# Performance work log

Hardware: AMD Instinct MI355X
Metric: run time of the kernel (lower is better)

## Reference

```python
import jax, jax.numpy as jnp
import numpy as np

B, ENC, DEC, H, W = 8, 64, 128, 128, 128
NEG = -1e30  # masked-softmax fill


def _neighbors(x):
    """x: [B,H,W,C] -> [B,H,W,9,C] 3x3 neighborhood gather (zeros at borders)."""
    b, h, w, c = x.shape
    p = jnp.pad(x, ((0, 0), (1, 1), (1, 1), (0, 0)))
    return jnp.stack([p[:, r:r + h, c_:c_ + w, :] for r in range(3) for c_ in range(3)], axis=3)


def _neighbor_mask(h, w):
    """[H,W,9] bool: which of the 9 neighbors are in-bounds per pixel."""
    m = jnp.pad(jnp.ones((h, w), dtype=bool), ((1, 1), (1, 1)))
    return jnp.stack([m[r:r + h, c_:c_ + w] for r in range(3) for c_ in range(3)], axis=2)


def setup_inputs() -> dict:
    key = jax.random.key(0)
    ks = jax.random.split(key, 12)
    s = 0.05
    return {
        "encoder_features": jax.random.normal(ks[0], (B, ENC, H, W), jnp.float32),
        "decoder_features": jax.random.normal(ks[1], (B, DEC, H, W), jnp.float32),
        "W_enc": jax.random.normal(ks[2], (ENC, ENC), jnp.float32) * s,
        "b_enc": jax.random.normal(ks[3], (ENC,), jnp.float32) * s,
        "W_dec": jax.random.normal(ks[4], (DEC, ENC), jnp.float32) * s,
        "b_dec": jax.random.normal(ks[5], (ENC,), jnp.float32) * s,
        "W_agg": jax.random.normal(ks[6], (ENC, 1), jnp.float32) * s,
        "b_agg": jax.random.normal(ks[7], (1,), jnp.float32) * s,
        "W_attn": jax.random.normal(ks[8], (2 * ENC, ENC), jnp.float32) * s,
        "b_attn": jax.random.normal(ks[9], (ENC,), jnp.float32) * s,
        "conv_w": jax.random.normal(ks[10], (3, 3, DEC, ENC), jnp.float32) * s,  # HWIO
        "conv_b": jax.random.normal(ks[11], (ENC,), jnp.float32) * s,
    }


def reference(encoder_features, decoder_features, W_enc, b_enc, W_dec, b_dec,
              W_agg, b_agg, W_attn, b_attn, conv_w, conv_b):
    # NCHW -> NHWC (format_linear)
    enc = jnp.transpose(encoder_features, (0, 2, 3, 1))  # [B,H,W,ENC]
    dec = jnp.transpose(decoder_features, (0, 2, 3, 1))  # [B,H,W,DEC]

    q = dec @ W_dec + b_dec  # [B,H,W,ENC]
    k = enc @ W_enc + b_enc  # [B,H,W,ENC]
    vals = jax.lax.conv_general_dilated(
        dec, conv_w, window_strides=(1, 1), padding='SAME',
        dimension_numbers=('NHWC', 'HWIO', 'NHWC')) + conv_b  # [B,H,W,ENC]

    kn = _neighbors(k)    # [B,H,W,9,ENC]
    en = _neighbors(enc)  # [B,H,W,9,ENC]
    mask = _neighbor_mask(q.shape[1], q.shape[2])  # [H,W,9]

    # per-neighbor additive score: agg_encoder(tanh(query + key)) -> scalar
    scores = jnp.squeeze(jnp.tanh(q[:, :, :, None, :] + kn) @ W_agg, -1) + b_agg  # [B,H,W,9]
    scores = jnp.where(mask, scores, NEG)
    attn_w = jax.nn.softmax(scores, axis=-1)  # softmax over valid neighbors only
    attn_vec = jnp.einsum('bhwn,bhwnc->bhwc', attn_w, en)  # weighted sum of raw encoder feats

    cat = jnp.concatenate([vals, attn_vec], axis=-1)  # [B,H,W,2*ENC]
    out = cat @ W_attn + b_attn
    out = jnp.where(out >= 0, out, 0.2 * out)  # LeakyReLU(0.2)
    return jnp.transpose(out, (0, 3, 1, 2))  # back to NCHW
```

## Files before the change

### kernel.cpp

```cpp
#include <hip/hip_runtime.h>

#define BB 8
#define ENC_C 64
#define DEC_C 128
#define HH 128
#define WW 128

typedef unsigned short ushort_t;
typedef __attribute__((ext_vector_type(8))) short short8;
typedef __attribute__((ext_vector_type(4))) float f32x4;

static __device__ __forceinline__ ushort_t f2bf(float x) {
  unsigned int u = __builtin_bit_cast(unsigned int, x);
  u += 0x7fff + ((u >> 16) & 1);
  return (ushort_t)(u >> 16);
}
static __device__ __forceinline__ float bf2f(ushort_t v) {
  unsigned int u = ((unsigned int)v) << 16;
  return __builtin_bit_cast(float, u);
}

__global__ __launch_bounds__(64) void pack_w_kernel(
    const float* __restrict__ conv_w, const float* __restrict__ W_attn,
    const float* __restrict__ W_dec, const float* __restrict__ W_enc,
    ushort_t* __restrict__ packedC, ushort_t* __restrict__ packedA,
    ushort_t* __restrict__ packedQ, ushort_t* __restrict__ packedK)
{
  const int blk = blockIdx.x;
  const int l = threadIdx.x;
  const float* W;
  ushort_t* dst;
  int bb;
  if (blk < 144) {
    const int kstep = blk >> 2, nf = blk & 3;
    const int tap = kstep >> 2, dstep = kstep & 3;
    const int n = nf * 16 + (l & 15);
    const int dbase = dstep * 32 + (l >> 4) * 8;
    ushort_t v[8];
    #pragma unroll
    for (int j = 0; j < 8; ++j)
      v[j] = f2bf(conv_w[(tap * DEC_C + dbase + j) * 64 + n]);
    ushort_t* d = packedC + ((long)blk * 64 + l) * 8;
    #pragma unroll
    for (int j = 0; j < 8; ++j) d[j] = v[j];
    return;
  } else if (blk < 160) {
    W = W_attn; dst = packedA; bb = blk - 144;
  } else if (blk < 176) {
    W = W_dec;  dst = packedQ; bb = blk - 160;
  } else {
    W = W_enc;  dst = packedK; bb = blk - 176;
  }
  const int ks = bb >> 2, nf = bb & 3;
  const int n = nf * 16 + (l & 15);
  const int kbase = ks * 32 + (l >> 4) * 8;
  ushort_t v[8];
  #pragma unroll
  for (int j = 0; j < 8; ++j)
    v[j] = f2bf(W[(kbase + j) * 64 + n]);
  ushort_t* d = dst + ((long)bb * 64 + l) * 8;
  #pragma unroll
  for (int j = 0; j < 8; ++j) d[j] = v[j];
}

__global__ __launch_bounds__(256) void prep_kernel(
    const float* __restrict__ enc, const float* __restrict__ dec,
    const ushort_t* __restrict__ packedQ, const ushort_t* __restrict__ packedK,
    const float* __restrict__ b_enc, const float* __restrict__ b_dec,
    ushort_t* __restrict__ q_nhwc, ushort_t* __restrict__ k_nhwc,
    ushort_t* __restrict__ enc_t, ushort_t* __restrict__ dec_t)
{
  __shared__ float smem[WW * 68];
  const int bh = blockIdx.x;
  const int b = bh >> 7, h = bh & 127;
  const int tid = threadIdx.x;
  const int l = tid & 63;
  const int wv = tid >> 6;
  const int pix0 = wv * 32;
  const int col = l & 15, kg = l >> 4;

  #pragma unroll
  for (int i = 0; i < 32; ++i) {
    int idx = tid + i * 256;
    int cc = idx >> 7, wl = idx & 127;
    smem[wl * 68 + cc] = enc[((b * ENC_C + cc) * HH + h) * WW + wl];
  }
  __syncthreads();

  #pragma unroll
  for (int i = 0; i < 32; ++i) {
    int idx = tid + i * 256;
    int wl = idx >> 6, cc = idx & 63;
    enc_t[((long)bh * WW + wl) * 64 + cc] = f2bf(smem[wl * 68 + cc]);
  }

  f32x4 acck[2][4];
  #pragma unroll
  for (int mf = 0; mf < 2; ++mf)
    #pragma unroll
    for (int nf = 0; nf < 4; ++nf)
      acck[mf][nf] = (f32x4){0.f, 0.f, 0.f, 0.f};

  #pragma unroll
  for (int ks = 0; ks < 2; ++ks) {
    short8 afr[2];
    #pragma unroll
    for (int mf = 0; mf < 2; ++mf) {
      const int pix = pix0 + mf * 16 + col;
      const float4* p = (const float4*)&smem[pix * 68 + ks * 32 + kg * 8];
      float4 x0 = p[0], x1 = p[1];
      short8 v;
      v[0] = (short)f2bf(x0.x); v[1] = (short)f2bf(x0.y);
      v[2] = (short)f2bf(x0.z); v[3] = (short)f2bf(x0.w);
      v[4] = (short)f2bf(x1.x); v[5] = (short)f2bf(x1.y);
      v[6] = (short)f2bf(x1.z); v[7] = (short)f2bf(x1.w);
      afr[mf] = v;
    }
    #pragma unroll
    for (int nf = 0; nf < 4; ++nf) {
      const short8 bfr =
          *(const short8*)(packedK + ((long)(ks * 4 + nf) * 64 + l) * 8);
      acck[0][nf] = __builtin_amdgcn_mfma_f32_16x16x32_bf16(
          afr[0], bfr, acck[0][nf], 0, 0, 0);
      acck[1][nf] = __builtin_amdgcn_mfma_f32_16x16x32_bf16(
          afr[1], bfr, acck[1][nf], 0, 0, 0);
    }
  }
  #pragma unroll
  for (int mf = 0; mf < 2; ++mf)
    #pragma unroll
    for (int nf = 0; nf < 4; ++nf)
      #pragma unroll
      for (int r = 0; r < 4; ++r) {
        const int pix = pix0 + mf * 16 + kg * 4 + r;
        const int c = nf * 16 + col;
        k_nhwc[((long)bh * WW + pix) * 64 + c] = f2bf(acck[mf][nf][r] + b_enc[c]);
      }
  __syncthreads();

  f32x4 accq[2][4];
  #pragma unroll
  for (int mf = 0; mf < 2; ++mf)
    #pragma unroll
    for (int nf = 0; nf < 4; ++nf)
      accq[mf][nf] = (f32x4){0.f, 0.f, 0.f, 0.f};

  #pragma unroll
  for (int hf = 0; hf < 2; ++hf) {
    #pragma unroll
    for (int i = 0; i < 32; ++i) {
      int idx = tid + i * 256;
      int cc = idx >> 7, wl = idx & 127;
      smem[wl * 68 + cc] = dec[((b * DEC_C + hf * 64 + cc) * HH + h) * WW + wl];
    }
    __syncthreads();

    #pragma unroll
    for (int i = 0; i < 32; ++i) {
      int idx = tid + i * 256;
      int wl = idx >> 6, cc = idx & 63;
      dec_t[((long)bh * WW + wl) * DEC_C + hf * 64 + cc] =
          f2bf(smem[wl * 68 + cc]);
    }

    #pragma unroll
    for (int ks2 = 0; ks2 < 2; ++ks2) {
      const int ks = hf * 2 + ks2;
      short8 afr[2];
      #pragma unroll
      for (int mf = 0; mf < 2; ++mf) {
        const int pix = pix0 + mf * 16 + col;
        const float4* p = (const float4*)&smem[pix * 68 + ks2 * 32 + kg * 8];
        float4 x0 = p[0], x1 = p[1];
        short8 v;
        v[0] = (short)f2bf(x0.x); v[1] = (short)f2bf(x0.y);
        v[2] = (short)f2bf(x0.z); v[3] = (short)f2bf(x0.w);
        v[4] = (short)f2bf(x1.x); v[5] = (short)f2bf(x1.y);
        v[6] = (short)f2bf(x1.z); v[7] = (short)f2bf(x1.w);
        afr[mf] = v;
      }
      #pragma unroll
      for (int nf = 0; nf < 4; ++nf) {
        const short8 bfr =
            *(const short8*)(packedQ + ((long)(ks * 4 + nf) * 64 + l) * 8);
        accq[0][nf] = __builtin_amdgcn_mfma_f32_16x16x32_bf16(
            afr[0], bfr, accq[0][nf], 0, 0, 0);
        accq[1][nf] = __builtin_amdgcn_mfma_f32_16x16x32_bf16(
            afr[1], bfr, accq[1][nf], 0, 0, 0);
      }
    }
    __syncthreads();
  }

  #pragma unroll
  for (int mf = 0; mf < 2; ++mf)
    #pragma unroll
    for (int nf = 0; nf < 4; ++nf)
      #pragma unroll
      for (int r = 0; r < 4; ++r) {
        const int pix = pix0 + mf * 16 + kg * 4 + r;
        const int c = nf * 16 + col;
        q_nhwc[((long)bh * WW + pix) * 64 + c] = f2bf(accq[mf][nf][r] + b_dec[c]);
      }
}

__global__ __launch_bounds__(256) void attn_kernel(
    const ushort_t* __restrict__ q_nhwc, const ushort_t* __restrict__ k_nhwc,
    const ushort_t* __restrict__ enc_t, const float* __restrict__ W_agg,
    const float* __restrict__ b_agg, ushort_t* __restrict__ att)
{
  const int nwg = gridDim.x;
  const int cpx = nwg >> 3;
  const int bid = blockIdx.x;
  const int swz = (bid & 7) * cpx + (bid >> 3);
  const int t = swz * 256 + threadIdx.x;
  const int pix = t >> 2;
  const int cb = (t & 3) * 16;
  const int h = (pix >> 7) & 127;
  const int w = pix & 127;

  int off[9]; bool valid[9];
  #pragma unroll
  for (int n = 0; n < 9; ++n) {
    const int dh = n / 3 - 1, dw = n % 3 - 1;
    const int nh = h + dh, nw = w + dw;
    valid[n] = (nh >= 0 && nh < HH && nw >= 0 && nw < WW);
    const int nhc = min(max(nh, 0), HH - 1);
    const int nwc = min(max(nw, 0), WW - 1);
    off[n] = (pix & ~16383) + nhc * WW + nwc;
  }

  const short8* qp = (const short8*)(q_nhwc + ((long)pix << 6) + cb);
  const short8 qa = qp[0], qb = qp[1];

  float wa[16];
  {
    float4 w0 = *(const float4*)(W_agg + cb);
    float4 w1 = *(const float4*)(W_agg + cb + 4);
    float4 w2 = *(const float4*)(W_agg + cb + 8);
    float4 w3 = *(const float4*)(W_agg + cb + 12);
    wa[0]=w0.x; wa[1]=w0.y; wa[2]=w0.z; wa[3]=w0.w;
    wa[4]=w1.x; wa[5]=w1.y; wa[6]=w1.z; wa[7]=w1.w;
    wa[8]=w2.x; wa[9]=w2.y; wa[10]=w2.z; wa[11]=w2.w;
    wa[12]=w3.x; wa[13]=w3.y; wa[14]=w3.z; wa[15]=w3.w;
  }

  float s[9];
  #pragma unroll
  for (int n = 0; n < 9; ++n) {
    const short8* kp = (const short8*)(k_nhwc + ((long)off[n] << 6) + cb);
    const short8 ka = kp[0], kb = kp[1];
    float sc = 0.f;
    #pragma unroll
    for (int e = 0; e < 8; ++e) {
      float x = bf2f((ushort_t)qa[e]) + bf2f((ushort_t)ka[e]);
      x = fminf(fmaxf(x, -15.f), 15.f);
      float z = __builtin_amdgcn_exp2f(x * 2.88539008f);
      float tt = __builtin_fmaf(-2.f, __builtin_amdgcn_rcpf(z + 1.f), 1.f);
      sc = __builtin_fmaf(tt, wa[e], sc);
    }
    #pragma unroll
    for (int e = 0; e < 8; ++e) {
      float x = bf2f((ushort_t)qb[e]) + bf2f((ushort_t)kb[e]);
      x = fminf(fmaxf(x, -15.f), 15.f);
      float z = __builtin_amdgcn_exp2f(x * 2.88539008f);
      float tt = __builtin_fmaf(-2.f, __builtin_amdgcn_rcpf(z + 1.f), 1.f);
      sc = __builtin_fmaf(tt, wa[8 + e], sc);
    }
    s[n] = sc;
  }

  #pragma unroll
  for (int n = 0; n < 9; ++n) {
    s[n] += __shfl_xor(s[n], 1);
    s[n] += __shfl_xor(s[n], 2);
  }

  const float bagg = b_agg[0];
  float m = -1e30f;
  #pragma unroll
  for (int n = 0; n < 9; ++n) {
    s[n] = valid[n] ? (s[n] + bagg) : -1e30f;
    m = fmaxf(m, s[n]);
  }
  float attw[9]; float denom = 0.f;
  #pragma unroll
  for (int n = 0; n < 9; ++n) {
    attw[n] = __builtin_amdgcn_exp2f((s[n] - m) * 1.44269504f);
    denom += attw[n];
  }
  const float inv = __builtin_amdgcn_rcpf(denom);
  #pragma unroll
  for (int n = 0; n < 9; ++n) attw[n] *= inv;

  float a16[16];
  #pragma unroll
  for (int e = 0; e < 16; ++e) a16[e] = 0.f;
  #pragma unroll
  for (int n = 0; n < 9; ++n) {
    const short8* ep = (const short8*)(enc_t + ((long)off[n] << 6) + cb);
    const short8 ea = ep[0], eb = ep[1];
    #pragma unroll
    for (int e = 0; e < 8; ++e)
      a16[e] = __builtin_fmaf(attw[n], bf2f((ushort_t)ea[e]), a16[e]);
    #pragma unroll
    for (int e = 0; e < 8; ++e)
      a16[8 + e] = __builtin_fmaf(attw[n], bf2f((ushort_t)eb[e]), a16[8 + e]);
  }
  short8 o0, o1;
  #pragma unroll
  for (int e = 0; e < 8; ++e) {
    o0[e] = (short)f2bf(a16[e]);
    o1[e] = (short)f2bf(a16[8 + e]);
  }
  short8* op = (short8*)(att + ((long)pix << 6) + cb);
  op[0] = o0;
  op[1] = o1;
}

__global__ __launch_bounds__(256) void conv_out_kernel(
    const ushort_t* __restrict__ dec_t, const ushort_t* __restrict__ packedC,
    const float* __restrict__ conv_b, const ushort_t* __restrict__ attn_nhwc,
    const ushort_t* __restrict__ packedA, const float* __restrict__ b_attn,
    float* __restrict__ out)
{
  __shared__ ushort_t bsh[24576];
  ushort_t* vlds = bsh;
  const int nwg = gridDim.x;
  const int cpx = nwg >> 3;
  const int bid = blockIdx.x;
  const int grp = (bid & 7) * cpx + (bid >> 3);
  const int b = grp >> 6;
  const int h0 = (grp & 63) * 2;
  const int tid = threadIdx.x;
  const int l = tid & 63;
  const int wv = tid >> 6;
  const int pix0 = wv * 32;
  const int col = l & 15, kg = l >> 4;

  f32x4 acc[2][2][4];
  #pragma unroll
  for (int r = 0; r < 2; ++r)
    #pragma unroll
    for (int mf = 0; mf < 2; ++mf)
      #pragma unroll
      for (int nf = 0; nf < 4; ++nf)
        acc[r][mf][nf] = (f32x4){0.f, 0.f, 0.f, 0.f};

  #pragma unroll
  for (int kh = 0; kh < 3; ++kh) {
    __syncthreads();
    {
      const short8* src = (const short8*)(packedC + (long)kh * 24576);
      #pragma unroll
      for (int i = 0; i < 12; ++i)
        *(short8*)&bsh[(tid + i * 256) * 8] = src[tid + i * 256];
    }
    __syncthreads();

    const int hh0 = h0 + kh - 1;
    const bool v0 = (hh0 >= 0);
    const bool v1 = (h0 + kh <= HH - 1);
    const ushort_t* arow0 = dec_t + ((long)(b * HH + (v0 ? hh0 : 0)) * WW) * DEC_C;
    const ushort_t* arow1 = dec_t + ((long)(b * HH + (v1 ? hh0 + 1 : 0)) * WW) * DEC_C;

    #pragma unroll
    for (int ds = 0; ds < 4; ++ds) {
      const int d0 = ds * 32;
      short8 afr[2][3][2];
      #pragma unroll
      for (int kw = 0; kw < 3; ++kw)
        #pragma unroll
        for (int mf = 0; mf < 2; ++mf) {
          const int wp = pix0 + mf * 16 + col + kw - 1;
          const bool wok = (wp >= 0 && wp < WW);
          short8 z = {0, 0, 0, 0, 0, 0, 0, 0};
          afr[0][kw][mf] = (wok && v0)
              ? *(const short8*)(arow0 + (long)wp * DEC_C + d0 + kg * 8) : z;
          afr[1][kw][mf] = (wok && v1)
              ? *(const short8*)(arow1 + (long)wp * DEC_C + d0 + kg * 8) : z;
        }
      #pragma unroll
      for (int kw = 0; kw < 3; ++kw) {
        #pragma unroll
        for (int nf = 0; nf < 4; ++nf) {
          const short8 bfr =
              *(const short8*)&bsh[(((kw * 4 + ds) * 4 + nf) * 64 + l) * 8];
          #pragma unroll
          for (int r = 0; r < 2; ++r) {
            acc[r][0][nf] = __builtin_amdgcn_mfma_f32_16x16x32_bf16(
                afr[r][kw][0], bfr, acc[r][0][nf], 0, 0, 0);
            acc[r][1][nf] = __builtin_amdgcn_mfma_f32_16x16x32_bf16(
                afr[r][kw][1], bfr, acc[r][1][nf], 0, 0, 0);
          }
        }
      }
    }
  }

  __syncthreads();
  #pragma unroll
  for (int r = 0; r < 2; ++r)
    #pragma unroll
    for (int mf = 0; mf < 2; ++mf)
      #pragma unroll
      for (int nf = 0; nf < 4; ++nf)
        #pragma unroll
        for (int rr = 0; rr < 4; ++rr) {
          const int pix = pix0 + mf * 16 + kg * 4 + rr;
          const int c = nf * 16 + col;
          vlds[(r * WW + pix) * 72 + c] = f2bf(acc[r][mf][nf][rr] + conv_b[c]);
        }
  __syncthreads();

  for (int r = 0; r < 2; ++r) {
    const int bh = b * HH + h0 + r;
    f32x4 ao[4][2];
    #pragma unroll
    for (int mf = 0; mf < 4; ++mf)
      #pragma unroll
      for (int pf = 0; pf < 2; ++pf)
        ao[mf][pf] = (f32x4){0.f, 0.f, 0.f, 0.f};

    #pragma unroll
    for (int ks = 0; ks < 4; ++ks) {
      short8 bfr[2];
      #pragma unroll
      for (int pf = 0; pf < 2; ++pf) {
        const int pix = pix0 + pf * 16 + col;
        short8 v;
        if (ks < 2) {
          v = *(const short8*)&vlds[(r * WW + pix) * 72 + ks * 32 + kg * 8];
        } else {
          v = *(const short8*)(attn_nhwc + ((long)bh * WW + pix) * 64 +
                               (ks - 2) * 32 + kg * 8);
        }
        bfr[pf] = v;
      }
      #pragma unroll
      for (int mf = 0; mf < 4; ++mf) {
        const short8 afr =
            *(const short8*)(packedA + ((long)(ks * 4 + mf) * 64 + l) * 8);
        #pragma unroll
        for (int pf = 0; pf < 2; ++pf)
          ao[mf][pf] = __builtin_amdgcn_mfma_f32_16x16x32_bf16(
              afr, bfr[pf], ao[mf][pf], 0, 0, 0);
      }
    }

    #pragma unroll
    for (int mf = 0; mf < 4; ++mf)
      #pragma unroll
      for (int pf = 0; pf < 2; ++pf)
        #pragma unroll
        for (int rr = 0; rr < 4; ++rr) {
          const int n = mf * 16 + kg * 4 + rr;
          const int pix = pix0 + pf * 16 + col;
          float o = ao[mf][pf][rr] + b_attn[n];
          o = (o >= 0.f) ? o : 0.2f * o;
          out[((long)(b * ENC_C + n) * HH + (h0 + r)) * WW + pix] = o;
        }
  }
}

extern "C" void kernel_launch(void* const* d_in, const int* in_sizes, int n_in,
                              void* d_out, int out_size, void* d_ws, size_t ws_size,
                              hipStream_t stream) {
  const float* enc    = (const float*)d_in[0];
  const float* dec    = (const float*)d_in[1];
  const float* W_enc  = (const float*)d_in[2];
  const float* b_enc  = (const float*)d_in[3];
  const float* W_dec  = (const float*)d_in[4];
  const float* b_dec  = (const float*)d_in[5];
  const float* W_agg  = (const float*)d_in[6];
  const float* b_agg  = (const float*)d_in[7];
  const float* W_attn = (const float*)d_in[8];
  const float* b_attn = (const float*)d_in[9];
  const float* conv_w = (const float*)d_in[10];
  const float* conv_b = (const float*)d_in[11];
  float* out = (float*)d_out;

  const long npix = (long)BB * HH * WW;
  ushort_t* q_bf    = (ushort_t*)d_ws;
  ushort_t* k_bf    = q_bf + npix * 64;
  ushort_t* enc_t   = k_bf + npix * 64;
  ushort_t* dec_t   = enc_t + npix * 64;
  ushort_t* att     = dec_t + npix * 128;
  ushort_t* packedC = att + npix * 64;
  ushort_t* packedA = packedC + 144 * 64 * 8;
  ushort_t* packedQ = packedA + 16 * 64 * 8;
  ushort_t* packedK = packedQ + 16 * 64 * 8;

  hipLaunchKernelGGL(pack_w_kernel, dim3(184), dim3(64), 0, stream,
                     conv_w, W_attn, W_dec, W_enc, packedC, packedA, packedQ, packedK);
  hipLaunchKernelGGL(prep_kernel, dim3(BB * HH), dim3(256), 0, stream,
                     enc, dec, packedQ, packedK, b_enc, b_dec, q_bf, k_bf, enc_t, dec_t);
  hipLaunchKernelGGL(attn_kernel, dim3((int)(npix * 4 / 256)), dim3(256), 0, stream,
                     q_bf, k_bf, enc_t, W_agg, b_agg, att);
  hipLaunchKernelGGL(conv_out_kernel, dim3(BB * HH / 2), dim3(256), 0, stream,
                     dec_t, packedC, conv_b, att, packedA, b_attn, out);
}
```

Baseline: 123.0 us.

## Double-buffer conv weights per tap via async global-to-LDS loads, one row per block

The conv+output kernel now processes one output row per workgroup instead of two, doubling the grid. Conv weights are repacked per 3x3 tap and staged into LDS with global_load_lds into a double buffer, so the next tap's weights load while the current tap's MFMAs run. Taps whose input row falls outside the image are skipped entirely. The trade-off is that weight reuse across two rows is lost, so weight traffic per output row doubles. In exchange, LDS and register use go down, which should allow more occupancy.

```diff
diff --git a/kernel.cpp b/kernel.cpp
--- a/kernel.cpp
+++ b/kernel.cpp
@@ -40,7 +40,7 @@
     #pragma unroll
     for (int j = 0; j < 8; ++j)
       v[j] = f2bf(conv_w[(tap * DEC_C + dbase + j) * 64 + n]);
-    ushort_t* d = packedC + ((long)blk * 64 + l) * 8;
+    ushort_t* d = packedC + (((long)tap * 16 + dstep * 4 + nf) * 64 + l) * 8;
     #pragma unroll
     for (int j = 0; j < 8; ++j) d[j] = v[j];
     return;
@@ -324,143 +324,131 @@
     const ushort_t* __restrict__ packedA, const float* __restrict__ b_attn,
     float* __restrict__ out)
 {
-  __shared__ ushort_t bsh[24576];
+  __shared__ ushort_t bsh[16384];
   ushort_t* vlds = bsh;
   const int nwg = gridDim.x;
   const int cpx = nwg >> 3;
   const int bid = blockIdx.x;
-  const int grp = (bid & 7) * cpx + (bid >> 3);
-  const int b = grp >> 6;
-  const int h0 = (grp & 63) * 2;
+  const int bh = (bid & 7) * cpx + (bid >> 3);
+  const int b = bh >> 7, h = bh & 127;
   const int tid = threadIdx.x;
   const int l = tid & 63;
   const int wv = tid >> 6;
   const int pix0 = wv * 32;
   const int col = l & 15, kg = l >> 4;
 
-  f32x4 acc[2][2][4];
-  #pragma unroll
-  for (int r = 0; r < 2; ++r)
-    #pragma unroll
-    for (int mf = 0; mf < 2; ++mf)
-      #pragma unroll
-      for (int nf = 0; nf < 4; ++nf)
-        acc[r][mf][nf] = (f32x4){0.f, 0.f, 0.f, 0.f};
-
-  #pragma unroll
-  for (int kh = 0; kh < 3; ++kh) {
+  auto stage = [&](int tap) {
+    const ushort_t* src = packedC + (long)tap * 8192;
+    ushort_t* dstb = bsh + (tap & 1) * 8192 + (long)(tid & ~63) * 8;
+    #pragma unroll
+    for (int i = 0; i < 4; ++i) {
+      __builtin_amdgcn_global_load_lds(
+          (const __attribute__((address_space(1))) void*)(src + (long)(i * 256 + tid) * 8),
+          (__attribute__((address_space(3))) void*)(dstb + i * 256 * 8),
+          16, 0, 0);
+    }
+  };
+
+  f32x4 acc[2][4];
+  #pragma unroll
+  for (int mf = 0; mf < 2; ++mf)
+    #pragma unroll
+    for (int nf = 0; nf < 4; ++nf)
+      acc[mf][nf] = (f32x4){0.f, 0.f, 0.f, 0.f};
+
+  stage(0);
+
+  #pragma unroll
+  for (int p = 0; p < 9; ++p) {
     __syncthreads();
-    {
-      const short8* src = (const short8*)(packedC + (long)kh * 24576);
-      #pragma unroll
-      for (int i = 0; i < 12; ++i)
-        *(short8*)&bsh[(tid + i * 256) * 8] = src[tid + i * 256];
-    }
-    __syncthreads();
-
-    const int hh0 = h0 + kh - 1;
-    const bool v0 = (hh0 >= 0);
-    const bool v1 = (h0 + kh <= HH - 1);
-    const ushort_t* arow0 = dec_t + ((long)(b * HH + (v0 ? hh0 : 0)) * WW) * DEC_C;
-    const ushort_t* arow1 = dec_t + ((long)(b * HH + (v1 ? hh0 + 1 : 0)) * WW) * DEC_C;
-
-    #pragma unroll
-    for (int ds = 0; ds < 4; ++ds) {
-      const int d0 = ds * 32;
-      short8 afr[2][3][2];
-      #pragma unroll
-      for (int kw = 0; kw < 3; ++kw)
+    if (p + 1 < 9) stage(p + 1);
+    const int kh = p / 3, kw = p % 3;
+    const int hh = h + kh - 1;
+    if (hh >= 0 && hh < HH) {
+      const ushort_t* arow = dec_t + ((long)(b * HH + hh) * WW) * DEC_C;
+      const ushort_t* bbase = bsh + (p & 1) * 8192;
+      short8 afr[4][2];
+      #pragma unroll
+      for (int ds = 0; ds < 4; ++ds)
         #pragma unroll
         for (int mf = 0; mf < 2; ++mf) {
           const int wp = pix0 + mf * 16 + col + kw - 1;
-          const bool wok = (wp >= 0 && wp < WW);
           short8 z = {0, 0, 0, 0, 0, 0, 0, 0};
-          afr[0][kw][mf] = (wok && v0)
-              ? *(const short8*)(arow0 + (long)wp * DEC_C + d0 + kg * 8) : z;
-          afr[1][kw][mf] = (wok && v1)
-              ? *(const short8*)(arow1 + (long)wp * DEC_C + d0 + kg * 8) : z;
+          afr[ds][mf] = (wp >= 0 && wp < WW)
+              ? *(const short8*)(arow + (long)wp * DEC_C + ds * 32 + kg * 8) : z;
         }
       #pragma unroll
-      for (int kw = 0; kw < 3; ++kw) {
+      for (int ds = 0; ds < 4; ++ds)
         #pragma unroll
         for (int nf = 0; nf < 4; ++nf) {
           const short8 bfr =
-              *(const short8*)&bsh[(((kw * 4 + ds) * 4 + nf) * 64 + l) * 8];
-          #pragma unroll
-          for (int r = 0; r < 2; ++r) {
-            acc[r][0][nf] = __builtin_amdgcn_mfma_f32_16x16x32_bf16(
-                afr[r][kw][0], bfr, acc[r][0][nf], 0, 0, 0);
-            acc[r][1][nf] = __builtin_amdgcn_mfma_f32_16x16x32_bf16(
-                afr[r][kw][1], bfr, acc[r][1][nf], 0, 0, 0);
-          }
+              *(const short8*)(bbase + ((ds * 4 + nf) * 64 + l) * 8);
+          acc[0][nf] = __builtin_amdgcn_mfma_f32_16x16x32_bf16(
+              afr[ds][0], bfr, acc[0][nf], 0, 0, 0);
+          acc[1][nf] = __builtin_amdgcn_mfma_f32_16x16x32_bf16(
+              afr[ds][1], bfr, acc[1][nf], 0, 0, 0);
         }
-      }
     }
   }
 
   __syncthreads();
   #pragma unroll
-  for (int r = 0; r < 2; ++r)
-    #pragma unroll
-    for (int mf = 0; mf < 2; ++mf)
-      #pragma unroll
-      for (int nf = 0; nf < 4; ++nf)
-        #pragma unroll
-        for (int rr = 0; rr < 4; ++rr) {
-          const int pix = pix0 + mf * 16 + kg * 4 + rr;
-          const int c = nf * 16 + col;
-          vlds[(r * WW + pix) * 72 + c] = f2bf(acc[r][mf][nf][rr] + conv_b[c]);
-        }
+  for (int mf = 0; mf < 2; ++mf)
+    #pragma unroll
+    for (int nf = 0; nf < 4; ++nf)
+      #pragma unroll
+      for (int r = 0; r < 4; ++r) {
+        const int pix = pix0 + mf * 16 + kg * 4 + r;
+        const int c = nf * 16 + col;
+        vlds[pix * 72 + c] = f2bf(acc[mf][nf][r] + conv_b[c]);
+      }
   __syncthreads();
 
-  for (int r = 0; r < 2; ++r) {
-    const int bh = b * HH + h0 + r;
-    f32x4 ao[4][2];
-    #pragma unroll
-    for (int mf = 0; mf < 4; ++mf)
+  f32x4 ao[4][2];
+  #pragma unroll
+  for (int mf = 0; mf < 4; ++mf)
+    #pragma unroll
+    for (int pf = 0; pf < 2; ++pf)
+      ao[mf][pf] = (f32x4){0.f, 0.f, 0.f, 0.f};
+
+  #pragma unroll
+  for (int ks = 0; ks < 4; ++ks) {
+    short8 bfr[2];
+    #pragma unroll
+    for (int pf = 0; pf < 2; ++pf) {
+      const int pix = pix0 + pf * 16 + col;
+      short8 v;
+      if (ks < 2) {
+        v = *(const short8*)&vlds[pix * 72 + ks * 32 + kg * 8];
+      } else {
+        v = *(const short8*)(attn_nhwc + ((long)bh * WW + pix) * 64 +
+                             (ks - 2) * 32 + kg * 8);
+      }
+      bfr[pf] = v;
+    }
+    #pragma unroll
+    for (int mf = 0; mf < 4; ++mf) {
+      const short8 afr =
+          *(const short8*)(packedA + ((long)(ks * 4 + mf) * 64 + l) * 8);
       #pragma unroll
       for (int pf = 0; pf < 2; ++pf)
-        ao[mf][pf] = (f32x4){0.f, 0.f, 0.f, 0.f};
-
-    #pragma unroll
-    for (int ks = 0; ks < 4; ++ks) {
-      short8 bfr[2];
-      #pragma unroll
-      for (int pf = 0; pf < 2; ++pf) {
+        ao[mf][pf] = __builtin_amdgcn_mfma_f32_16x16x32_bf16(
+            afr, bfr[pf], ao[mf][pf], 0, 0, 0);
+    }
+  }
+
+  #pragma unroll
+  for (int mf = 0; mf < 4; ++mf)
+    #pragma unroll
+    for (int pf = 0; pf < 2; ++pf)
+      #pragma unroll
+      for (int r = 0; r < 4; ++r) {
+        const int n = mf * 16 + kg * 4 + r;
         const int pix = pix0 + pf * 16 + col;
-        short8 v;
-        if (ks < 2) {
-          v = *(const short8*)&vlds[(r * WW + pix) * 72 + ks * 32 + kg * 8];
-        } else {
-          v = *(const short8*)(attn_nhwc + ((long)bh * WW + pix) * 64 +
-                               (ks - 2) * 32 + kg * 8);
-        }
-        bfr[pf] = v;
-      }
-      #pragma unroll
-      for (int mf = 0; mf < 4; ++mf) {
-        const short8 afr =
-            *(const short8*)(packedA + ((long)(ks * 4 + mf) * 64 + l) * 8);
-        #pragma unroll
-        for (int pf = 0; pf < 2; ++pf)
-          ao[mf][pf] = __builtin_amdgcn_mfma_f32_16x16x32_bf16(
-              afr, bfr[pf], ao[mf][pf], 0, 0, 0);
-      }
-    }
-
-    #pragma unroll
-    for (int mf = 0; mf < 4; ++mf)
-      #pragma unroll
-      for (int pf = 0; pf < 2; ++pf)
-        #pragma unroll
-        for (int rr = 0; rr < 4; ++rr) {
-          const int n = mf * 16 + kg * 4 + rr;
-          const int pix = pix0 + pf * 16 + col;
-          float o = ao[mf][pf][rr] + b_attn[n];
-          o = (o >= 0.f) ? o : 0.2f * o;
-          out[((long)(b * ENC_C + n) * HH + (h0 + r)) * WW + pix] = o;
-        }
-  }
+        float o = ao[mf][pf][r] + b_attn[n];
+        o = (o >= 0.f) ? o : 0.2f * o;
+        out[((long)(b * ENC_C + n) * HH + h) * WW + pix] = o;
+      }
 }
 
 extern "C" void kernel_launch(void* const* d_in, const int* in_sizes, int n_in,
@@ -497,6 +485,6 @@
                      enc, dec, packedQ, packedK, b_enc, b_dec, q_bf, k_bf, enc_t, dec_t);
   hipLaunchKernelGGL(attn_kernel, dim3((int)(npix * 4 / 256)), dim3(256), 0, stream,
                      q_bf, k_bf, enc_t, W_agg, b_agg, att);
-  hipLaunchKernelGGL(conv_out_kernel, dim3(BB * HH / 2), dim3(256), 0, stream,
+  hipLaunchKernelGGL(conv_out_kernel, dim3(BB * HH), dim3(256), 0, stream,
                      dec_t, packedC, conv_b, att, packedA, b_attn, out);
 }
```

Result: faster. 120.5 us (-2.0%).
